# Kernel tuning notes

Measured on AMD Instinct MI355X. Metric: run time of the kernel, lower is better.

## Reference

```python
import jax, jax.numpy as jnp
import numpy as np

S, B, H = 2048, 32, 1024

def setup_inputs() -> dict:
    key = jax.random.key(0)
    k1, k2, k3, k4, k5 = jax.random.split(key, 5)
    hidden = jax.random.normal(k1, (B, H), dtype=jnp.float32)
    encoder_outputs = jax.random.normal(k2, (S, B, 2 * H), dtype=jnp.float32)
    # nn.Linear(3H, H): weight [H, 3H] in torch; store transposed [3H, H] for x @ W
    W = jax.random.normal(k3, (3 * H, H), dtype=jnp.float32) * (1.0 / np.sqrt(3 * H))
    b = jax.random.normal(k4, (H,), dtype=jnp.float32) * 0.01
    v = jax.random.uniform(k5, (H,), dtype=jnp.float32)  # torch.rand
    return {"hidden": hidden, "encoder_outputs": encoder_outputs, "W": W, "b": b, "v": v}

def reference(hidden, encoder_outputs, W, b, v):
    # hidden: [B, H]; encoder_outputs: [S, B, 2H]
    # Avoid materializing the repeated/concatenated tensor by splitting the linear:
    # cat(h_rep, enc) @ W == h @ W[:H] (broadcast over S) + enc @ W[H:]
    Wh, We = W[:H], W[H:]                         # [H, H], [2H, H]
    h_proj = hidden @ Wh + b                      # [B, H]
    energy = jnp.tanh(jnp.einsum('sbe,eh->sbh', encoder_outputs, We) + h_proj[None])  # [S, B, H]
    scores = jnp.einsum('sbh,h->bs', energy, v)   # [B, S]
    return jax.nn.softmax(scores, axis=1)
```

## Files before the change

### kernel.cpp

```cpp
#include <hip/hip_runtime.h>
#include <hip/hip_fp16.h>


typedef _Float16 half8 __attribute__((ext_vector_type(8)));
typedef float floatx4 __attribute__((ext_vector_type(4)));
typedef float f32x4 __attribute__((ext_vector_type(4)));

constexpr int SEQ = 2048;
constexpr int BAT = 32;
constexpr int HID = 1024;
constexpr int KDIM = 2048;
constexpr int MTOT = SEQ * BAT;
constexpr int KT = 64;

constexpr int B_BUF = 65536;
constexpr int A_PITCH = 64 * 16 + 16;
constexpr int A_BUF = 4 * A_PITCH;

__device__ __forceinline__ void glds16(const void* g, void* l) {
    __builtin_amdgcn_global_load_lds((__attribute__((address_space(1))) void*)(g),
                                     (__attribute__((address_space(3))) void*)(l), 16, 0, 0);
}

__global__ __launch_bounds__(256) void pack_b_kernel(const float* __restrict__ W,
                                                     _Float16* __restrict__ pb) {
    int t = blockIdx.x * blockDim.x + threadIdx.x;
    int nt = t >> 15;
    int rem = t & 32767;
    int kt = rem >> 9;
    int c = rem & 511;
    int g = c >> 7;
    int n = c & 127;
    int h = nt * 128 + n;
    int e0 = kt * 32 + g * 8;
    const float* src = W + (size_t)(1024 + e0) * 1024 + h;
    union { _Float16 hh[8]; uint4 u; } tmp;
#pragma unroll
    for (int j = 0; j < 8; ++j) tmp.hh[j] = (_Float16)src[(size_t)j * 1024];
    *(uint4*)(pb + (size_t)t * 8) = tmp.u;
}

__global__ __launch_bounds__(256) void hproj_kernel(const float* __restrict__ hidden,
                                                    const float* __restrict__ W,
                                                    const float* __restrict__ bias,
                                                    float* __restrict__ hp) {
    int b = blockIdx.x;
    int h0 = blockIdx.y * 64;
    int hl = threadIdx.x & 63;
    int ks = threadIdx.x >> 6;
    const float* hr = hidden + b * HID + ks * 256;
    const float* wc = W + (size_t)(ks * 256) * HID + h0 + hl;
    float acc = 0.0f;
#pragma unroll 8
    for (int e = 0; e < 256; ++e) acc += hr[e] * wc[(size_t)e * HID];
    __shared__ float red[256];
    red[threadIdx.x] = acc;
    __syncthreads();
    if (threadIdx.x < 64)
        hp[b * HID + h0 + threadIdx.x] = red[threadIdx.x] + red[64 + threadIdx.x] +
                                         red[128 + threadIdx.x] + red[192 + threadIdx.x] +
                                         bias[h0 + threadIdx.x];
}

__global__ __launch_bounds__(512, 2) void attn_gemm_kernel(
    const float* __restrict__ enc, const _Float16* __restrict__ pb,
    const float* __restrict__ hp, const float* __restrict__ v,
    float* __restrict__ score) {
    __shared__ char smem[2 * B_BUF + 2 * A_BUF];
    char* sB0 = smem;
    char* sB1 = smem + B_BUF;
    char* sA0 = smem + 2 * B_BUF;
    char* sA1 = smem + 2 * B_BUF + A_BUF;

    const int tid = threadIdx.x;
    const int lane = tid & 63;
    const int wv = tid >> 6;
    const int mt = blockIdx.x;
    const size_t r0 = (size_t)mt * 64;
    const int fm = lane & 15;
    const int fg = lane >> 4;

    const char* bg = (const char*)pb + (size_t)wv * KT * 8192;
    const int bl_off = wv * 8192;

    const int arow = tid >> 3;
    const int ac4 = tid & 7;
    const f32x4* agp = (const f32x4*)(enc + (r0 + arow) * KDIM) + ac4;
    const int awoff = (ac4 >> 1) * A_PITCH + arow * 16 + (ac4 & 1) * 8;

    const int ardoff = fg * A_PITCH + fm * 16;
    const int brdoff = wv * 8192 + fg * 2048 + fm * 16;

    floatx4 acc[4][8];
#pragma unroll
    for (int i = 0; i < 4; ++i)
#pragma unroll
        for (int j = 0; j < 8; ++j) acc[i][j] = (floatx4)0.0f;

    {
        const char* g = bg;
        char* l0 = sB0 + bl_off;
#pragma unroll
        for (int j = 0; j < 8; ++j)
            glds16(g + (j * 64 + lane) * 16, l0 + (j * 64 + lane) * 16);
        f32x4 f = __builtin_nontemporal_load(agp);
        union { _Float16 hh[4]; uint2 u; } pk;
        pk.hh[0] = (_Float16)f.x; pk.hh[1] = (_Float16)f.y;
        pk.hh[2] = (_Float16)f.z; pk.hh[3] = (_Float16)f.w;
        *(uint2*)(sA0 + awoff) = pk.u;
    }

    for (int kt = 0; kt < KT; ++kt) {
        const int cur = kt & 1;
        __syncthreads();
        if (kt + 1 < KT) {
            char* sBn = (cur ? sB0 : sB1);
            char* sAn = (cur ? sA0 : sA1);
            const char* g = bg + (size_t)(kt + 1) * 8192;
            char* l0 = sBn + bl_off;
#pragma unroll
            for (int j = 0; j < 8; ++j)
                glds16(g + (j * 64 + lane) * 16, l0 + (j * 64 + lane) * 16);
            f32x4 f = __builtin_nontemporal_load(agp + (kt + 1) * 8);
            union { _Float16 hh[4]; uint2 u; } pk;
            pk.hh[0] = (_Float16)f.x; pk.hh[1] = (_Float16)f.y;
            pk.hh[2] = (_Float16)f.z; pk.hh[3] = (_Float16)f.w;
            *(uint2*)(sAn + awoff) = pk.u;
        }
        const char* ab = cur ? sA1 : sA0;
        const char* bb = cur ? sB1 : sB0;
        half8 af[4];
#pragma unroll
        for (int i = 0; i < 4; ++i) af[i] = *(const half8*)(ab + ardoff + i * 256);
#pragma unroll
        for (int j = 0; j < 8; ++j) {
            half8 bf = *(const half8*)(bb + brdoff + j * 256);
#pragma unroll
            for (int i = 0; i < 4; ++i)
                acc[i][j] = __builtin_amdgcn_mfma_f32_16x16x32_f16(af[i], bf, acc[i][j], 0, 0, 0);
        }
    }

    float sums[4][4];
#pragma unroll
    for (int i = 0; i < 4; ++i)
#pragma unroll
        for (int r = 0; r < 4; ++r) sums[i][r] = 0.0f;

#pragma unroll
    for (int j = 0; j < 8; ++j) {
        int h = wv * 128 + j * 16 + fm;
        float vv = v[h];
#pragma unroll
        for (int i = 0; i < 4; ++i) {
#pragma unroll
            for (int r = 0; r < 4; ++r) {
                int row = i * 16 + fg * 4 + r;
                int b = row & 31;
                float x = acc[i][j][r] + hp[b * HID + h];
                float e2 = __expf(2.0f * x);
                float th = 1.0f - 2.0f / (e2 + 1.0f);
                sums[i][r] += th * vv;
            }
        }
    }
#pragma unroll
    for (int i = 0; i < 4; ++i)
#pragma unroll
        for (int r = 0; r < 4; ++r) {
            float s = sums[i][r];
            s += __shfl_xor(s, 1);
            s += __shfl_xor(s, 2);
            s += __shfl_xor(s, 4);
            s += __shfl_xor(s, 8);
            sums[i][r] = s;
        }
    __syncthreads();
    float* red = (float*)smem;
    if (fm == 0) {
#pragma unroll
        for (int i = 0; i < 4; ++i)
#pragma unroll
            for (int r = 0; r < 4; ++r)
                red[wv * 64 + i * 16 + fg * 4 + r] = sums[i][r];
    }
    __syncthreads();
    if (tid < 64) {
        float tot = 0.0f;
#pragma unroll
        for (int w = 0; w < 8; ++w) tot += red[w * 64 + tid];
        score[r0 + tid] = tot;
    }
}

__global__ __launch_bounds__(256) void softmax_kernel(const float* __restrict__ score,
                                                      float* __restrict__ out) {
    int b = blockIdx.x;
    int tid = threadIdx.x;
    __shared__ float redm[4];
    __shared__ float reds[4];
    float vals[8];
    float mx = -1e30f;
#pragma unroll
    for (int k = 0; k < 8; ++k) {
        int s = k * 256 + tid;
        float a = score[(size_t)s * 32 + b];
        vals[k] = a;
        mx = fmaxf(mx, a);
    }
    for (int d = 1; d < 64; d <<= 1) mx = fmaxf(mx, __shfl_xor(mx, d));
    int wv = tid >> 6;
    if ((tid & 63) == 0) redm[wv] = mx;
    __syncthreads();
    mx = fmaxf(fmaxf(redm[0], redm[1]), fmaxf(redm[2], redm[3]));
    float sum = 0.0f;
#pragma unroll
    for (int k = 0; k < 8; ++k) {
        vals[k] = __expf(vals[k] - mx);
        sum += vals[k];
    }
    for (int d = 1; d < 64; d <<= 1) sum += __shfl_xor(sum, d);
    if ((tid & 63) == 0) reds[wv] = sum;
    __syncthreads();
    sum = reds[0] + reds[1] + reds[2] + reds[3];
    float inv = 1.0f / sum;
#pragma unroll
    for (int k = 0; k < 8; ++k) out[b * SEQ + k * 256 + tid] = vals[k] * inv;
}

extern "C" void kernel_launch(void* const* d_in, const int* in_sizes, int n_in,
                              void* d_out, int out_size, void* d_ws, size_t ws_size,
                              hipStream_t stream) {
    const float* hidden = (const float*)d_in[0];
    const float* enc    = (const float*)d_in[1];
    const float* W      = (const float*)d_in[2];
    const float* bias   = (const float*)d_in[3];
    const float* v      = (const float*)d_in[4];
    float* out = (float*)d_out;

    char* ws = (char*)d_ws;
    _Float16* packB = (_Float16*)ws;
    float* hp       = (float*)(ws + (4u << 20));
    float* score    = (float*)(ws + (4u << 20) + (128u << 10));

    pack_b_kernel<<<1024, 256, 0, stream>>>(W, packB);
    hproj_kernel<<<dim3(32, 16), 256, 0, stream>>>(hidden, W, bias, hp);
    attn_gemm_kernel<<<MTOT / 64, 512, 0, stream>>>(enc, packB, hp, v, score);
    softmax_kernel<<<BAT, 256, 0, stream>>>(score, out);
}
```

Before: 1.075 ms.

## Load B fragments directly from global memory instead of staging through LDS

Removes the 128 KB double-buffered LDS staging of the packed weight tiles. Each wave now reads its own B fragments straight from global memory (L2-resident packed fp16) into registers every k-step. The encoder loads also switch from nontemporal to ordinary loads. This shrinks LDS use to the small A buffers, which could allow more resident blocks, but it puts global-load latency directly in front of the MFMAs with no prefetch and adds register pressure.

New measurement: 1.456 ms. +35.5%, slower.

```diff
diff --git a/kernel.cpp b/kernel.cpp
--- a/kernel.cpp
+++ b/kernel.cpp
@@ -13,14 +13,8 @@
 constexpr int MTOT = SEQ * BAT;
 constexpr int KT = 64;
 
-constexpr int B_BUF = 65536;
 constexpr int A_PITCH = 64 * 16 + 16;
 constexpr int A_BUF = 4 * A_PITCH;
-
-__device__ __forceinline__ void glds16(const void* g, void* l) {
-    __builtin_amdgcn_global_load_lds((__attribute__((address_space(1))) void*)(g),
-                                     (__attribute__((address_space(3))) void*)(l), 16, 0, 0);
-}
 
 __global__ __launch_bounds__(256) void pack_b_kernel(const float* __restrict__ W,
                                                      _Float16* __restrict__ pb) {
@@ -66,11 +60,9 @@
     const float* __restrict__ enc, const _Float16* __restrict__ pb,
     const float* __restrict__ hp, const float* __restrict__ v,
     float* __restrict__ score) {
-    __shared__ char smem[2 * B_BUF + 2 * A_BUF];
-    char* sB0 = smem;
-    char* sB1 = smem + B_BUF;
-    char* sA0 = smem + 2 * B_BUF;
-    char* sA1 = smem + 2 * B_BUF + A_BUF;
+    __shared__ char smem[2 * A_BUF];
+    char* sA0 = smem;
+    char* sA1 = smem + A_BUF;
 
     const int tid = threadIdx.x;
     const int lane = tid & 63;
@@ -80,16 +72,14 @@
     const int fm = lane & 15;
     const int fg = lane >> 4;
 
-    const char* bg = (const char*)pb + (size_t)wv * KT * 8192;
-    const int bl_off = wv * 8192;
-
     const int arow = tid >> 3;
     const int ac4 = tid & 7;
     const f32x4* agp = (const f32x4*)(enc + (r0 + arow) * KDIM) + ac4;
     const int awoff = (ac4 >> 1) * A_PITCH + arow * 16 + (ac4 & 1) * 8;
 
+    const char* bp = (const char*)pb + (size_t)wv * KT * 8192 + fg * 2048 + fm * 16;
+
     const int ardoff = fg * A_PITCH + fm * 16;
-    const int brdoff = wv * 8192 + fg * 2048 + fm * 16;
 
     floatx4 acc[4][8];
 #pragma unroll
@@ -98,12 +88,7 @@
         for (int j = 0; j < 8; ++j) acc[i][j] = (floatx4)0.0f;
 
     {
-        const char* g = bg;
-        char* l0 = sB0 + bl_off;
-#pragma unroll
-        for (int j = 0; j < 8; ++j)
-            glds16(g + (j * 64 + lane) * 16, l0 + (j * 64 + lane) * 16);
-        f32x4 f = __builtin_nontemporal_load(agp);
+        f32x4 f = *agp;
         union { _Float16 hh[4]; uint2 u; } pk;
         pk.hh[0] = (_Float16)f.x; pk.hh[1] = (_Float16)f.y;
         pk.hh[2] = (_Float16)f.z; pk.hh[3] = (_Float16)f.w;
@@ -113,32 +98,30 @@
     for (int kt = 0; kt < KT; ++kt) {
         const int cur = kt & 1;
         __syncthreads();
+        const char* ab = cur ? sA1 : sA0;
+        const char* bk = bp + (size_t)kt * 8192;
+
+        half8 af[4];
+#pragma unroll
+        for (int i = 0; i < 4; ++i) af[i] = *(const half8*)(ab + ardoff + i * 256);
+
+        half8 bf[8];
+#pragma unroll
+        for (int j = 0; j < 8; ++j) bf[j] = *(const half8*)(bk + j * 256);
+
         if (kt + 1 < KT) {
-            char* sBn = (cur ? sB0 : sB1);
-            char* sAn = (cur ? sA0 : sA1);
-            const char* g = bg + (size_t)(kt + 1) * 8192;
-            char* l0 = sBn + bl_off;
-#pragma unroll
-            for (int j = 0; j < 8; ++j)
-                glds16(g + (j * 64 + lane) * 16, l0 + (j * 64 + lane) * 16);
-            f32x4 f = __builtin_nontemporal_load(agp + (kt + 1) * 8);
+            f32x4 f = agp[(kt + 1) * 8];
             union { _Float16 hh[4]; uint2 u; } pk;
             pk.hh[0] = (_Float16)f.x; pk.hh[1] = (_Float16)f.y;
             pk.hh[2] = (_Float16)f.z; pk.hh[3] = (_Float16)f.w;
-            *(uint2*)(sAn + awoff) = pk.u;
+            *(uint2*)((cur ? sA0 : sA1) + awoff) = pk.u;
         }
-        const char* ab = cur ? sA1 : sA0;
-        const char* bb = cur ? sB1 : sB0;
-        half8 af[4];
-#pragma unroll
-        for (int i = 0; i < 4; ++i) af[i] = *(const half8*)(ab + ardoff + i * 256);
-#pragma unroll
-        for (int j = 0; j < 8; ++j) {
-            half8 bf = *(const half8*)(bb + brdoff + j * 256);
+
+#pragma unroll
+        for (int j = 0; j < 8; ++j)
 #pragma unroll
             for (int i = 0; i < 4; ++i)
-                acc[i][j] = __builtin_amdgcn_mfma_f32_16x16x32_f16(af[i], bf, acc[i][j], 0, 0, 0);
-        }
+                acc[i][j] = __builtin_amdgcn_mfma_f32_16x16x32_f16(af[i], bf[j], acc[i][j], 0, 0, 0);
     }
 
     float sums[4][4];
```
